# Kernel optimization log

Hardware: AMD Instinct MI355X
Metric: run time of the kernel (lower is better)

## Reference

```python
import jax, jax.numpy as jnp
import numpy as np

D_MODEL = 1024
N_HEADS = 16
D_V = D_MODEL // N_HEADS  # 64


def setup_inputs() -> dict:
    key = jax.random.key(0)
    k1, k2, k3, k4, k5, k6 = jax.random.split(key, 6)
    N, L = 2, 2048
    return {
        "queries": jax.random.normal(k1, (N, L, D_MODEL), jnp.float32),
        "keys": jax.random.normal(k2, (N, L, D_MODEL), jnp.float32),
        "values": jax.random.normal(k3, (N, L, D_MODEL), jnp.float32),
        # key-padding mask, 0 = masked out (broadcast over heads and queries)
        "mask": jax.random.randint(k4, (N, 1, 1, L), 0, 2).astype(jnp.int32),
        # torch nn.Linear(d_model, d_model): weight [out, in], bias [out]
        "fc_w": jax.random.normal(k5, (D_MODEL, D_MODEL), jnp.float32) / np.sqrt(D_MODEL).astype(np.float32),
        "fc_b": jax.random.normal(k6, (D_MODEL,), jnp.float32) * 0.01,
    }


def reference(queries, keys, values, mask, fc_w, fc_b):
    N, Lq, _ = queries.shape
    Lk = keys.shape[1]
    # NOTE: the source defines Q/K/V Linear layers but never applies them in forward.
    q = queries.reshape(N, Lq, N_HEADS, D_V).transpose(0, 2, 1, 3)  # [N,H,Lq,Dv]
    k = keys.reshape(N, Lk, N_HEADS, D_V)                            # [N,Lk,H,Dv]
    v = values.reshape(N, Lk, N_HEADS, D_V)                          # [N,Lk,H,Dv]
    energy = jnp.einsum('nhqd,nkhd->nhqk', q, k)                     # QK^T
    energy = jnp.where(mask == 0, -jnp.inf, energy)                  # masked_fill
    # faithful to source: scale by sqrt(d_model), applied after masking
    attn = jax.nn.softmax(energy / jnp.sqrt(jnp.float32(D_MODEL)), axis=-1)
    out = jnp.einsum('nhqk,nkhd->nqhd', attn, v).reshape(N, Lq, N_HEADS * D_V)
    return out @ fc_w.T + fc_b
```

## Files before the change

### kernel.cpp

```cpp
#include <hip/hip_runtime.h>

#define SEQL 2048
#define DMODEL 1024

typedef short bf16x8 __attribute__((ext_vector_type(8)));
typedef short bf16x4 __attribute__((ext_vector_type(4)));
typedef float f32x4 __attribute__((ext_vector_type(4)));
typedef unsigned short u16;

__device__ __forceinline__ u16 f2bf(float f) {
    union { float f; unsigned u; } v; v.f = f;
    unsigned r = v.u + 0x7FFFu + ((v.u >> 16) & 1u);
    return (u16)(r >> 16);
}

__global__ __launch_bounds__(256) void pack_all(
    const float* __restrict__ kg, const float* __restrict__ wg,
    const float* __restrict__ vg, const int* __restrict__ mg,
    u16* __restrict__ kb, u16* __restrict__ wb, u16* __restrict__ vtb,
    float* __restrict__ maskf)
{
    __shared__ __align__(16) u16 T[64 * 72];
    const int b = blockIdx.x, t = threadIdx.x;
    u16 o[8];
    if (b < 2048) {
        const int e0 = (b * 256 + t) * 8;
        const int n = e0 >> 21, rem = e0 & ((1 << 21) - 1);
        const int s = rem >> 10, dm = rem & 1023, h = dm >> 6, d = dm & 63;
        const float4 x0 = *(const float4*)(kg + e0);
        const float4 x1 = *(const float4*)(kg + e0 + 4);
        o[0]=f2bf(x0.x); o[1]=f2bf(x0.y); o[2]=f2bf(x0.z); o[3]=f2bf(x0.w);
        o[4]=f2bf(x1.x); o[5]=f2bf(x1.y); o[6]=f2bf(x1.z); o[7]=f2bf(x1.w);
        *(bf16x8*)(kb + ((((size_t)n * 16 + h) * 2048 + s) * 64 + d)) = *(bf16x8*)o;
    } else if (b < 2560) {
        const int e0 = ((b - 2048) * 256 + t) * 8;
        const float4 x0 = *(const float4*)(wg + e0);
        const float4 x1 = *(const float4*)(wg + e0 + 4);
        o[0]=f2bf(x0.x); o[1]=f2bf(x0.y); o[2]=f2bf(x0.z); o[3]=f2bf(x0.w);
        o[4]=f2bf(x1.x); o[5]=f2bf(x1.y); o[6]=f2bf(x1.z); o[7]=f2bf(x1.w);
        *(bf16x8*)(wb + e0) = *(bf16x8*)o;
    } else if (b < 3584) {
        const int bb = b - 2560;
        const int st = bb & 31, h = (bb >> 5) & 15, n = bb >> 9;
        {
            const int s = t >> 2, d0 = (t & 3) * 16;
            const float* src = vg + ((size_t)(n * SEQL + st * 64 + s) * DMODEL) + h * 64 + d0;
            u16 w16[16];
            #pragma unroll
            for (int j = 0; j < 16; ++j) w16[j] = f2bf(src[j]);
            *(bf16x8*)&T[s * 72 + d0]     = *(bf16x8*)&w16[0];
            *(bf16x8*)&T[s * 72 + d0 + 8] = *(bf16x8*)&w16[8];
        }
        __syncthreads();
        {
            const int d = t >> 2, k0 = (t & 3) * 16;
            u16 w16[16];
            #pragma unroll
            for (int j = 0; j < 16; ++j) w16[j] = T[(k0 + j) * 72 + d];
            u16* dst = vtb + ((size_t)((n * 16 + h) * 64 + d) * SEQL) + st * 64 + k0;
            *(bf16x8*)dst       = *(bf16x8*)&w16[0];
            *(bf16x8*)(dst + 8) = *(bf16x8*)&w16[8];
        }
    } else {
        #pragma unroll
        for (int i = 0; i < 16; ++i) {
            const int idx = t * 16 + i;
            maskf[idx] = mg[idx] ? 1.0f : 0.0f;
        }
    }
}

#define KSTR 72
#define VSTR 72
#define PT 72
#define OSPLIT 4194304
#define LSPLIT 65536

template<int NSPLIT>
__global__ __launch_bounds__(256) void attn_kernel(
    const float* __restrict__ qg, const u16* __restrict__ kb,
    const u16* __restrict__ vtb, const float* __restrict__ maskf,
    u16* __restrict__ xb, float* __restrict__ opart, float* __restrict__ lpart)
{
    __shared__ __align__(16) u16 K_lds[64 * KSTR];
    __shared__ __align__(16) u16 Vt_lds[64 * VSTR];
    __shared__ __align__(16) u16 P_lds[128 * PT];

    const int blk = blockIdx.x;
    const int qblk = blk & 15;
    const int h = (blk >> 4) & 15;
    const int n = (blk >> 8) & 1;
    const int split = blk >> 9;
    const int tid = threadIdx.x;
    const int wave = tid >> 6, lane = tid & 63;
    const int lrow = lane & 15, quad = lane >> 4;
    const int q0 = qblk * 128;

    bf16x8 qf[2][2];
    #pragma unroll
    for (int qi = 0; qi < 2; ++qi) {
        const float* qp = qg + ((size_t)(n * SEQL + q0 + wave * 32 + qi * 16 + lrow) * DMODEL) + h * 64 + quad * 8;
        #pragma unroll
        for (int f = 0; f < 2; ++f) {
            const float4 a = *(const float4*)(qp + f * 32);
            const float4 c = *(const float4*)(qp + f * 32 + 4);
            u16* dst = (u16*)&qf[qi][f];
            dst[0]=f2bf(a.x); dst[1]=f2bf(a.y); dst[2]=f2bf(a.z); dst[3]=f2bf(a.w);
            dst[4]=f2bf(c.x); dst[5]=f2bf(c.y); dst[6]=f2bf(c.z); dst[7]=f2bf(c.w);
        }
    }

    bf16x8 onesf;
    #pragma unroll
    for (int j = 0; j < 8; ++j) ((u16*)&onesf)[j] = 0x3F80;

    f32x4 oacc[2][4];
    f32x4 lacc[2];
    #pragma unroll
    for (int qi = 0; qi < 2; ++qi) {
        lacc[qi] = (f32x4){0.f, 0.f, 0.f, 0.f};
        #pragma unroll
        for (int t4 = 0; t4 < 4; ++t4) oacc[qi][t4] = (f32x4){0.f, 0.f, 0.f, 0.f};
    }

    const u16* ksrc0 = kb  + ((size_t)(n * 16 + h) * SEQL) * 64;
    const u16* vsrc0 = vtb + ((size_t)(n * 16 + h) * 64) * SEQL;
    const float* mrow = maskf + n * SEQL;

    const int ktlo = split * (32 / NSPLIT);
    const int kthi = ktlo + (32 / NSPLIT);

    for (int kt = ktlo; kt < kthi; ++kt) {
        __syncthreads();
        {
            const u16* ks = ksrc0 + (size_t)kt * 64 * 64;
            const u16* vs = vsrc0 + kt * 64;
            #pragma unroll
            for (int i = 0; i < 2; ++i) {
                const int c = tid + i * 256;
                const int r = c >> 3, e0 = (c & 7) * 8;
                *(bf16x8*)&K_lds[r * KSTR + e0]  = *(const bf16x8*)(ks + c * 8);
                *(bf16x8*)&Vt_lds[r * VSTR + e0] = *(const bf16x8*)(vs + (size_t)r * SEQL + e0);
            }
        }
        __syncthreads();

        #pragma unroll
        for (int st = 0; st < 4; ++st) {
            const bf16x8 kf0 = *(const bf16x8*)&K_lds[(st * 16 + lrow) * KSTR + quad * 8];
            const bf16x8 kf1 = *(const bf16x8*)&K_lds[(st * 16 + lrow) * KSTR + 32 + quad * 8];
            const f32x4 mv = *(const f32x4*)&mrow[kt * 64 + st * 16 + quad * 4];
            #pragma unroll
            for (int qi = 0; qi < 2; ++qi) {
                f32x4 sa = (f32x4){0.f, 0.f, 0.f, 0.f};
                sa = __builtin_amdgcn_mfma_f32_16x16x32_bf16(kf0, qf[qi][0], sa, 0, 0, 0);
                sa = __builtin_amdgcn_mfma_f32_16x16x32_bf16(kf1, qf[qi][1], sa, 0, 0, 0);
                u16 p[4];
                #pragma unroll
                for (int r = 0; r < 4; ++r)
                    p[r] = f2bf(mv[r] * __expf(sa[r] * 0.03125f));
                *(bf16x4*)&P_lds[(wave * 32 + qi * 16 + lrow) * PT + st * 16 + quad * 4] = *(bf16x4*)p;
            }
        }
        asm volatile("s_waitcnt lgkmcnt(0)" ::: "memory");

        bf16x8 vf[4][2];
        #pragma unroll
        for (int t4 = 0; t4 < 4; ++t4) {
            vf[t4][0] = *(const bf16x8*)&Vt_lds[(t4 * 16 + lrow) * VSTR + quad * 8];
            vf[t4][1] = *(const bf16x8*)&Vt_lds[(t4 * 16 + lrow) * VSTR + 32 + quad * 8];
        }
        #pragma unroll
        for (int qi = 0; qi < 2; ++qi) {
            const int prow = (wave * 32 + qi * 16 + lrow) * PT;
            const bf16x8 pf0 = *(const bf16x8*)&P_lds[prow + quad * 8];
            const bf16x8 pf1 = *(const bf16x8*)&P_lds[prow + 32 + quad * 8];
            lacc[qi] = __builtin_amdgcn_mfma_f32_16x16x32_bf16(pf0, onesf, lacc[qi], 0, 0, 0);
            lacc[qi] = __builtin_amdgcn_mfma_f32_16x16x32_bf16(pf1, onesf, lacc[qi], 0, 0, 0);
            #pragma unroll
            for (int t4 = 0; t4 < 4; ++t4) {
                oacc[qi][t4] = __builtin_amdgcn_mfma_f32_16x16x32_bf16(pf0, vf[t4][0], oacc[qi][t4], 0, 0, 0);
                oacc[qi][t4] = __builtin_amdgcn_mfma_f32_16x16x32_bf16(pf1, vf[t4][1], oacc[qi][t4], 0, 0, 0);
            }
        }
    }

    if (NSPLIT == 1) {
        #pragma unroll
        for (int qi = 0; qi < 2; ++qi)
            #pragma unroll
            for (int r = 0; r < 4; ++r) {
                const float rinv = 1.0f / lacc[qi][r];
                const int q = q0 + wave * 32 + qi * 16 + quad * 4 + r;
                u16* op = xb + (size_t)(n * SEQL + q) * DMODEL + h * 64 + lrow;
                #pragma unroll
                for (int t4 = 0; t4 < 4; ++t4)
                    op[t4 * 16] = f2bf(oacc[qi][t4][r] * rinv);
            }
    } else {
        #pragma unroll
        for (int qi = 0; qi < 2; ++qi) {
            #pragma unroll
            for (int r = 0; r < 4; ++r) {
                const int q = q0 + wave * 32 + qi * 16 + quad * 4 + r;
                float* op = opart + (size_t)split * OSPLIT + (size_t)(n * SEQL + q) * DMODEL + h * 64 + lrow;
                #pragma unroll
                for (int t4 = 0; t4 < 4; ++t4)
                    op[t4 * 16] = oacc[qi][t4][r];
                if (lrow == 0)
                    lpart[split * LSPLIT + (n * SEQL + q) * 16 + h] = lacc[qi][r];
            }
        }
    }
}

__global__ __launch_bounds__(256) void reduce_norm(
    const float* __restrict__ opart, const float* __restrict__ lpart,
    u16* __restrict__ xb)
{
    const int gid = blockIdx.x * 256 + threadIdx.x;
    const int e0 = gid * 8;
    const int row = e0 >> 10, c = e0 & 1023, h = c >> 6;
    const float rinv = 1.0f / (lpart[row * 16 + h] + lpart[LSPLIT + row * 16 + h]);
    const float4 a0 = *(const float4*)(opart + e0);
    const float4 a1 = *(const float4*)(opart + e0 + 4);
    const float4 b0 = *(const float4*)(opart + OSPLIT + e0);
    const float4 b1 = *(const float4*)(opart + OSPLIT + e0 + 4);
    u16 o[8];
    o[0] = f2bf((a0.x + b0.x) * rinv); o[1] = f2bf((a0.y + b0.y) * rinv);
    o[2] = f2bf((a0.z + b0.z) * rinv); o[3] = f2bf((a0.w + b0.w) * rinv);
    o[4] = f2bf((a1.x + b1.x) * rinv); o[5] = f2bf((a1.y + b1.y) * rinv);
    o[6] = f2bf((a1.z + b1.z) * rinv); o[7] = f2bf((a1.w + b1.w) * rinv);
    *(bf16x8*)(xb + e0) = *(bf16x8*)o;
}

#define FSTR 72

__global__ __launch_bounds__(256) void fc_kernel(
    const u16* __restrict__ xb, const u16* __restrict__ wb,
    const float* __restrict__ bias, float* __restrict__ out)
{
    __shared__ __align__(16) u16 X_lds[128 * FSTR];
    __shared__ __align__(16) u16 W_lds[128 * FSTR];

    const int blk = blockIdx.x;
    const int cb = blk & 7, rb = blk >> 3;
    const int row0 = rb * 128, col0 = cb * 128;
    const int tid = threadIdx.x;
    const int wave = tid >> 6, lane = tid & 63;
    const int lrow = lane & 15, quad = lane >> 4;

    f32x4 acc[2][8];
    #pragma unroll
    for (int ri = 0; ri < 2; ++ri)
        #pragma unroll
        for (int cj = 0; cj < 8; ++cj) acc[ri][cj] = (f32x4){0.f, 0.f, 0.f, 0.f};

    for (int kt = 0; kt < 16; ++kt) {
        __syncthreads();
        #pragma unroll
        for (int i = 0; i < 4; ++i) {
            const int idx = tid + i * 256;
            const int r = idx >> 3, e0 = (idx & 7) * 8;
            *(bf16x8*)&X_lds[r * FSTR + e0] = *(const bf16x8*)(xb + (size_t)(row0 + r) * DMODEL + kt * 64 + e0);
            *(bf16x8*)&W_lds[r * FSTR + e0] = *(const bf16x8*)(wb + (size_t)(col0 + r) * DMODEL + kt * 64 + e0);
        }
        __syncthreads();

        bf16x8 af[2][2];
        #pragma unroll
        for (int ri = 0; ri < 2; ++ri) {
            af[ri][0] = *(const bf16x8*)&X_lds[(wave * 32 + ri * 16 + lrow) * FSTR + quad * 8];
            af[ri][1] = *(const bf16x8*)&X_lds[(wave * 32 + ri * 16 + lrow) * FSTR + 32 + quad * 8];
        }
        #pragma unroll
        for (int cj = 0; cj < 8; ++cj) {
            const bf16x8 bf0 = *(const bf16x8*)&W_lds[(cj * 16 + lrow) * FSTR + quad * 8];
            const bf16x8 bf1 = *(const bf16x8*)&W_lds[(cj * 16 + lrow) * FSTR + 32 + quad * 8];
            #pragma unroll
            for (int ri = 0; ri < 2; ++ri) {
                acc[ri][cj] = __builtin_amdgcn_mfma_f32_16x16x32_bf16(af[ri][0], bf0, acc[ri][cj], 0, 0, 0);
                acc[ri][cj] = __builtin_amdgcn_mfma_f32_16x16x32_bf16(af[ri][1], bf1, acc[ri][cj], 0, 0, 0);
            }
        }
    }

    #pragma unroll
    for (int ri = 0; ri < 2; ++ri)
        #pragma unroll
        for (int cj = 0; cj < 8; ++cj) {
            const int col = col0 + cj * 16 + lrow;
            const float bv = bias[col];
            #pragma unroll
            for (int r = 0; r < 4; ++r)
                out[(size_t)(row0 + wave * 32 + ri * 16 + quad * 4 + r) * DMODEL + col] = acc[ri][cj][r] + bv;
        }
}

extern "C" void kernel_launch(void* const* d_in, const int* in_sizes, int n_in,
                              void* d_out, int out_size, void* d_ws, size_t ws_size,
                              hipStream_t stream) {
    const float* q   = (const float*)d_in[0];
    const float* k   = (const float*)d_in[1];
    const float* v   = (const float*)d_in[2];
    const int*   m   = (const int*)d_in[3];
    const float* fcw = (const float*)d_in[4];
    const float* fcb = (const float*)d_in[5];
    float* out = (float*)d_out;

    char* ws = (char*)d_ws;
    u16*   kbuf  = (u16*)(ws);
    u16*   vtbuf = (u16*)(ws + (8u  << 20));
    u16*   wbuf  = (u16*)(ws + (16u << 20));
    u16*   xbuf  = (u16*)(ws + (18u << 20));
    float* maskf = (float*)(ws + (26u << 20));
    float* opart = (float*)(ws + (27u << 20));
    float* lpart = (float*)(ws + (59u << 20));
    const bool split2 = ws_size >= (60u << 20);

    pack_all<<<dim3(3585), dim3(256), 0, stream>>>(k, fcw, v, m, kbuf, wbuf, vtbuf, maskf);
    if (split2) {
        attn_kernel<2><<<dim3(1024), dim3(256), 0, stream>>>(q, kbuf, vtbuf, maskf, xbuf, opart, lpart);
        reduce_norm<<<dim3(2048), dim3(256), 0, stream>>>(opart, lpart, xbuf);
    } else {
        attn_kernel<1><<<dim3(512), dim3(256), 0, stream>>>(q, kbuf, vtbuf, maskf, xbuf, opart, lpart);
    }
    fc_kernel<<<dim3(256), dim3(256), 0, stream>>>(xbuf, wbuf, fcb, out);
}
```

Baseline: 193.0 us.

## Fuse split-reduce normalization into FC GEMM, use additive mask, narrow FC tile

Removes the separate reduce_norm kernel. The FC kernel now reads both fp32 attention partials and the row sums directly, then normalizes and converts to bf16 while filling its LDS tile. The FC output tile shrinks from 128x128 to 128x64, so the grid grows to 512 blocks. The mask becomes an additive bias inside the exp via fma, and the bf16 packing uses hardware conversion intrinsics. The cost is that each FC block re-reads the fp32 partials for its rows, so the wider fp32 X traffic is repeated across 16 column blocks.

```diff
diff --git a/kernel.cpp b/kernel.cpp
--- a/kernel.cpp
+++ b/kernel.cpp
@@ -1,4 +1,5 @@
 #include <hip/hip_runtime.h>
+#include <hip/hip_bf16.h>
 
 #define SEQL 2048
 #define DMODEL 1024
@@ -65,7 +66,7 @@
         #pragma unroll
         for (int i = 0; i < 16; ++i) {
             const int idx = t * 16 + i;
-            maskf[idx] = mg[idx] ? 1.0f : 0.0f;
+            maskf[idx] = mg[idx] ? 0.0f : -1.0e5f;
         }
     }
 }
@@ -155,11 +156,16 @@
                 f32x4 sa = (f32x4){0.f, 0.f, 0.f, 0.f};
                 sa = __builtin_amdgcn_mfma_f32_16x16x32_bf16(kf0, qf[qi][0], sa, 0, 0, 0);
                 sa = __builtin_amdgcn_mfma_f32_16x16x32_bf16(kf1, qf[qi][1], sa, 0, 0, 0);
-                u16 p[4];
-                #pragma unroll
-                for (int r = 0; r < 4; ++r)
-                    p[r] = f2bf(mv[r] * __expf(sa[r] * 0.03125f));
-                *(bf16x4*)&P_lds[(wave * 32 + qi * 16 + lrow) * PT + st * 16 + quad * 4] = *(bf16x4*)p;
+                float e0v = __expf(fmaf(sa[0], 0.03125f, mv[0]));
+                float e1v = __expf(fmaf(sa[1], 0.03125f, mv[1]));
+                float e2v = __expf(fmaf(sa[2], 0.03125f, mv[2]));
+                float e3v = __expf(fmaf(sa[3], 0.03125f, mv[3]));
+                __hip_bfloat162 h0 = __float22bfloat162_rn(make_float2(e0v, e1v));
+                __hip_bfloat162 h1 = __float22bfloat162_rn(make_float2(e2v, e3v));
+                union { unsigned u[2]; bf16x4 v; } pk;
+                pk.u[0] = *(unsigned*)&h0;
+                pk.u[1] = *(unsigned*)&h1;
+                *(bf16x4*)&P_lds[(wave * 32 + qi * 16 + lrow) * PT + st * 16 + quad * 4] = pk.v;
             }
         }
         asm volatile("s_waitcnt lgkmcnt(0)" ::: "memory");
@@ -214,56 +220,61 @@
     }
 }
 
-__global__ __launch_bounds__(256) void reduce_norm(
-    const float* __restrict__ opart, const float* __restrict__ lpart,
-    u16* __restrict__ xb)
-{
-    const int gid = blockIdx.x * 256 + threadIdx.x;
-    const int e0 = gid * 8;
-    const int row = e0 >> 10, c = e0 & 1023, h = c >> 6;
-    const float rinv = 1.0f / (lpart[row * 16 + h] + lpart[LSPLIT + row * 16 + h]);
-    const float4 a0 = *(const float4*)(opart + e0);
-    const float4 a1 = *(const float4*)(opart + e0 + 4);
-    const float4 b0 = *(const float4*)(opart + OSPLIT + e0);
-    const float4 b1 = *(const float4*)(opart + OSPLIT + e0 + 4);
-    u16 o[8];
-    o[0] = f2bf((a0.x + b0.x) * rinv); o[1] = f2bf((a0.y + b0.y) * rinv);
-    o[2] = f2bf((a0.z + b0.z) * rinv); o[3] = f2bf((a0.w + b0.w) * rinv);
-    o[4] = f2bf((a1.x + b1.x) * rinv); o[5] = f2bf((a1.y + b1.y) * rinv);
-    o[6] = f2bf((a1.z + b1.z) * rinv); o[7] = f2bf((a1.w + b1.w) * rinv);
-    *(bf16x8*)(xb + e0) = *(bf16x8*)o;
-}
-
 #define FSTR 72
 
+template<bool FUSED>
 __global__ __launch_bounds__(256) void fc_kernel(
-    const u16* __restrict__ xb, const u16* __restrict__ wb,
+    const u16* __restrict__ xb, const float* __restrict__ opart,
+    const float* __restrict__ lpart, const u16* __restrict__ wb,
     const float* __restrict__ bias, float* __restrict__ out)
 {
     __shared__ __align__(16) u16 X_lds[128 * FSTR];
-    __shared__ __align__(16) u16 W_lds[128 * FSTR];
+    __shared__ __align__(16) u16 W_lds[64 * FSTR];
 
     const int blk = blockIdx.x;
-    const int cb = blk & 7, rb = blk >> 3;
-    const int row0 = rb * 128, col0 = cb * 128;
+    const int cb = blk & 15, rb = blk >> 4;
+    const int row0 = rb * 128, col0 = cb * 64;
     const int tid = threadIdx.x;
     const int wave = tid >> 6, lane = tid & 63;
     const int lrow = lane & 15, quad = lane >> 4;
 
-    f32x4 acc[2][8];
+    f32x4 acc[2][4];
     #pragma unroll
     for (int ri = 0; ri < 2; ++ri)
         #pragma unroll
-        for (int cj = 0; cj < 8; ++cj) acc[ri][cj] = (f32x4){0.f, 0.f, 0.f, 0.f};
+        for (int cj = 0; cj < 4; ++cj) acc[ri][cj] = (f32x4){0.f, 0.f, 0.f, 0.f};
 
     for (int kt = 0; kt < 16; ++kt) {
         __syncthreads();
         #pragma unroll
         for (int i = 0; i < 4; ++i) {
-            const int idx = tid + i * 256;
-            const int r = idx >> 3, e0 = (idx & 7) * 8;
-            *(bf16x8*)&X_lds[r * FSTR + e0] = *(const bf16x8*)(xb + (size_t)(row0 + r) * DMODEL + kt * 64 + e0);
-            *(bf16x8*)&W_lds[r * FSTR + e0] = *(const bf16x8*)(wb + (size_t)(col0 + r) * DMODEL + kt * 64 + e0);
+            const int g = tid + i * 256;
+            const int r = g >> 3, e0 = (g & 7) * 8;
+            if (FUSED) {
+                const float* p0 = opart + (size_t)(row0 + r) * DMODEL + kt * 64 + e0;
+                const float4 a0 = *(const float4*)p0;
+                const float4 a1 = *(const float4*)(p0 + 4);
+                const float4 b0 = *(const float4*)(p0 + OSPLIT);
+                const float4 b1 = *(const float4*)(p0 + OSPLIT + 4);
+                const float ri_ = __frcp_rn(lpart[(row0 + r) * 16 + kt] +
+                                            lpart[LSPLIT + (row0 + r) * 16 + kt]);
+                u16 o[8];
+                o[0] = f2bf((a0.x + b0.x) * ri_); o[1] = f2bf((a0.y + b0.y) * ri_);
+                o[2] = f2bf((a0.z + b0.z) * ri_); o[3] = f2bf((a0.w + b0.w) * ri_);
+                o[4] = f2bf((a1.x + b1.x) * ri_); o[5] = f2bf((a1.y + b1.y) * ri_);
+                o[6] = f2bf((a1.z + b1.z) * ri_); o[7] = f2bf((a1.w + b1.w) * ri_);
+                *(bf16x8*)&X_lds[r * FSTR + e0] = *(bf16x8*)o;
+            } else {
+                *(bf16x8*)&X_lds[r * FSTR + e0] =
+                    *(const bf16x8*)(xb + (size_t)(row0 + r) * DMODEL + kt * 64 + e0);
+            }
+        }
+        #pragma unroll
+        for (int i = 0; i < 2; ++i) {
+            const int g = tid + i * 256;
+            const int r = g >> 3, e0 = (g & 7) * 8;
+            *(bf16x8*)&W_lds[r * FSTR + e0] =
+                *(const bf16x8*)(wb + (size_t)(col0 + r) * DMODEL + kt * 64 + e0);
         }
         __syncthreads();
 
@@ -274,7 +285,7 @@
             af[ri][1] = *(const bf16x8*)&X_lds[(wave * 32 + ri * 16 + lrow) * FSTR + 32 + quad * 8];
         }
         #pragma unroll
-        for (int cj = 0; cj < 8; ++cj) {
+        for (int cj = 0; cj < 4; ++cj) {
             const bf16x8 bf0 = *(const bf16x8*)&W_lds[(cj * 16 + lrow) * FSTR + quad * 8];
             const bf16x8 bf1 = *(const bf16x8*)&W_lds[(cj * 16 + lrow) * FSTR + 32 + quad * 8];
             #pragma unroll
@@ -288,7 +299,7 @@
     #pragma unroll
     for (int ri = 0; ri < 2; ++ri)
         #pragma unroll
-        for (int cj = 0; cj < 8; ++cj) {
+        for (int cj = 0; cj < 4; ++cj) {
             const int col = col0 + cj * 16 + lrow;
             const float bv = bias[col];
             #pragma unroll
@@ -321,9 +332,9 @@
     pack_all<<<dim3(3585), dim3(256), 0, stream>>>(k, fcw, v, m, kbuf, wbuf, vtbuf, maskf);
     if (split2) {
         attn_kernel<2><<<dim3(1024), dim3(256), 0, stream>>>(q, kbuf, vtbuf, maskf, xbuf, opart, lpart);
-        reduce_norm<<<dim3(2048), dim3(256), 0, stream>>>(opart, lpart, xbuf);
+        fc_kernel<true><<<dim3(512), dim3(256), 0, stream>>>(xbuf, opart, lpart, wbuf, fcb, out);
     } else {
         attn_kernel<1><<<dim3(512), dim3(256), 0, stream>>>(q, kbuf, vtbuf, maskf, xbuf, opart, lpart);
-    }
-    fc_kernel<<<dim3(256), dim3(256), 0, stream>>>(xbuf, wbuf, fcb, out);
-}
+        fc_kernel<false><<<dim3(512), dim3(256), 0, stream>>>(xbuf, opart, lpart, wbuf, fcb, out);
+    }
+}
```

Measured after the change: 221.1 us. +14.5%, slower.
